# Performance work log

Hardware: AMD Instinct MI355X
Metric: run time of the kernel (lower is better)

The kernel has to match this reference:

```python
import jax, jax.numpy as jnp
import numpy as np

C = 64
SIZE = 448
PATCH = 14
P2 = PATCH * PATCH                 # 196, per-chunk token count
SPLIT = (SIZE * SIZE) // P2        # 1024 chunks
TG = PATCH * 4                     # 56, pooled global resolution
POOL = SIZE // TG                  # 8, exact avg-pool factor
EPS = 1e-5


def setup_inputs() -> dict:
    key = jax.random.key(0)
    ks = jax.random.split(key, 10)
    b = 2
    x = jax.random.normal(ks[0], (b, C, SIZE, SIZE), dtype=jnp.float32)
    s = 1.0 / np.sqrt(C)
    return {
        "x": x,
        "gn_w": jnp.ones((C,), jnp.float32),
        "gn_b": jnp.zeros((C,), jnp.float32),
        "q_w": jax.random.normal(ks[1], (C, C), jnp.float32) * s,
        "q_b": jnp.zeros((C,), jnp.float32),
        "k_w": jax.random.normal(ks[2], (C, C), jnp.float32) * s,
        "k_b": jnp.zeros((C,), jnp.float32),
        "v_w": jax.random.normal(ks[3], (C, C), jnp.float32) * s,
        "v_b": jnp.zeros((C,), jnp.float32),
        "proj_w": jax.random.normal(ks[4], (C, C), jnp.float32) * s,
    }


def _conv1x1(t, W, bias=None):
    out = jnp.einsum('oc,bchw->bohw', W, t)
    if bias is not None:
        out = out + bias[None, :, None, None]
    return out


def _group_norm(x, w, b):
    # GroupNorm(num_groups=1): normalize over (C,H,W) per sample
    mean = x.mean(axis=(1, 2, 3), keepdims=True)
    var = x.var(axis=(1, 2, 3), keepdims=True)
    xn = (x - mean) * jax.lax.rsqrt(var + EPS)
    return xn * w[None, :, None, None] + b[None, :, None, None]


def reference(x, gn_w, gn_b, q_w, q_b, k_w, k_b, v_w, v_b, proj_w):
    b, c, h, w = x.shape
    xn = _group_norm(x, gn_w, gn_b)
    q = _conv1x1(xn, q_w, q_b)
    k = _conv1x1(xn, k_w, k_b)
    v = _conv1x1(xn, v_w, v_b)

    # ---- patch-local attention (channels*chunks as feature dim S) ----
    S = c * SPLIT  # 65536
    qf = q.reshape(b, S, P2)
    kf = k.reshape(b, S, P2)
    vf = v.reshape(b, S, P2)
    wm = jnp.einsum('bsp,bsq->bpq', qf, kf) * (S ** -0.5)  # [b,196,196]
    wm = jax.nn.softmax(wm, axis=2)
    # h[b,s,q'] = sum_k v[b,s,k] * wm[b,q',k]
    hp = jnp.einsum('bsk,bqk->bsq', vf, wm).reshape(b, c, h, w)

    # ---- global pooled attention ----
    pool = lambda t: t.reshape(b, c, TG, POOL, TG, POOL).mean(axis=(3, 5))
    qg = pool(q).reshape(b, c, TG * TG)
    kg = pool(k).reshape(b, c, TG * TG)
    vg = pool(v).reshape(b, c, TG * TG)
    wg = jnp.einsum('bcp,bcq->bpq', qg, kg) * (c ** -0.5)  # [b,3136,3136]
    wg = jax.nn.softmax(wg, axis=2)
    hg = jnp.einsum('bck,bqk->bcq', vg, wg).reshape(b, c, TG, TG)
    hg = jnp.repeat(jnp.repeat(hg, POOL, axis=2), POOL, axis=3)

    h_in = 0.75 * hp + 0.25 * hg
    out = _conv1x1(h_in, proj_w)  # proj_out, no bias
    return x + out
```

## Files before the change

### kernel.cpp

```cpp
#include <hip/hip_runtime.h>

#define NB 2
#define NC 64
#define HW 200704
#define CHW 12845056
#define P2 196
#define NCHUNK 1024
#define NCELL 3136
#define WMN 38416

typedef __attribute__((ext_vector_type(8))) short bfrag;
typedef __attribute__((ext_vector_type(4))) float ffrag;
typedef __attribute__((ext_vector_type(4))) short short4v;
typedef __attribute__((ext_vector_type(4))) float float4v;

#define MFMA16(A,B,C) __builtin_amdgcn_mfma_f32_16x16x32_bf16(A,B,C,0,0,0)

__device__ __forceinline__ short f2bf(float f) {
  unsigned u = __builtin_bit_cast(unsigned, f);
  u = u + 0x7FFFu + ((u >> 16) & 1u);
  return (short)(u >> 16);
}

__global__ __launch_bounds__(256) void k0_fold(
    const float* __restrict__ pw, const float* __restrict__ vw,
    const float* __restrict__ vb, float* __restrict__ wtld, float* __restrict__ btld) {
  int t = threadIdx.x;
  if (blockIdx.x == 0) {
    #pragma unroll
    for (int i = 0; i < 16; ++i) {
      int idx = i*256 + t;
      int o = idx >> 6, c = idx & 63;
      float s = 0.f;
      for (int m = 0; m < 64; ++m) s += pw[o*64 + m] * vw[m*64 + c];
      wtld[o*64 + c] = s;
    }
  } else {
    if (t < 64) {
      float s = 0.f;
      for (int m = 0; m < 64; ++m) s += pw[t*64 + m] * vb[m];
      btld[t] = s;
    }
  }
}

__global__ __launch_bounds__(64) void k1_stats_pool(
    const float* __restrict__ x, float* __restrict__ xpool, float* __restrict__ partials) {
  int bx = blockIdx.x;
  int batch = bx / (64*56);
  int c = (bx / 56) % 64;
  int pr = bx % 56;
  int l = threadIdx.x;
  const float* xp = x + (size_t)batch*CHW + (size_t)c*HW + pr*8*448;
  float cell = 0.f, s2 = 0.f;
  if (l < 56) {
    #pragma unroll
    for (int r = 0; r < 8; ++r) {
      float4v a = *(const float4v*)(xp + r*448 + l*8);
      float4v b = *(const float4v*)(xp + r*448 + l*8 + 4);
      #pragma unroll
      for (int j = 0; j < 4; ++j) { cell += a[j] + b[j]; s2 += a[j]*a[j] + b[j]*b[j]; }
    }
    xpool[((size_t)batch*64 + c)*NCELL + pr*56 + l] = cell * (1.f/64.f);
  }
  float s1 = (l < 56) ? cell : 0.f;
  #pragma unroll
  for (int m = 1; m < 64; m <<= 1) { s1 += __shfl_xor(s1, m, 64); s2 += __shfl_xor(s2, m, 64); }
  if (l == 0) { partials[bx*2] = s1; partials[bx*2 + 1] = s2; }
}

__global__ __launch_bounds__(256) void k1b_reduce(
    const float* __restrict__ partials, float* __restrict__ stats) {
  __shared__ float red[2][256];
  int t = threadIdx.x;
  for (int b = 0; b < NB; ++b) {
    float s1 = 0.f, s2 = 0.f;
    for (int i = t; i < 3584; i += 256) {
      s1 += partials[(b*3584 + i)*2];
      s2 += partials[(b*3584 + i)*2 + 1];
    }
    red[0][t] = s1; red[1][t] = s2;
    __syncthreads();
    for (int m = 128; m > 0; m >>= 1) {
      if (t < m) { red[0][t] += red[0][t+m]; red[1][t] += red[1][t+m]; }
      __syncthreads();
    }
    if (t == 0) { stats[b*2] = red[0][0]; stats[b*2+1] = red[1][0]; }
    __syncthreads();
  }
}

__global__ __launch_bounds__(256) void k2_qkv(
    const float* __restrict__ x, const float* __restrict__ gnw, const float* __restrict__ gnb,
    const float* __restrict__ qw, const float* __restrict__ qb,
    const float* __restrict__ kw, const float* __restrict__ kb,
    const float* __restrict__ vw, const float* __restrict__ vb,
    const float* __restrict__ stats,
    short* __restrict__ qx, short* __restrict__ kx, short* __restrict__ vnat) {
  __shared__ __attribute__((aligned(16))) short xnt[256*72];
  int bx = blockIdx.x;
  int batch = bx / 784;
  int px0 = (bx % 784) * 256;
  int t = threadIdx.x;
  float s1 = stats[batch*2], s2 = stats[batch*2+1];
  float mean = s1 * (1.f/CHW);
  float rstd = rsqrtf(s2*(1.f/CHW) - mean*mean + 1e-5f);
  for (int it = 0; it < 64; it += 4) {
    float vv[4];
    #pragma unroll
    for (int r = 0; r < 4; ++r) {
      float v = x[(size_t)batch*CHW + (size_t)(it+r)*HW + px0 + t];
      vv[r] = (v - mean) * rstd * gnw[it+r] + gnb[it+r];
    }
    short4v s;
    #pragma unroll
    for (int r = 0; r < 4; ++r) s[r] = f2bf(vv[r]);
    *(short4v*)(xnt + t*72 + it) = s;
  }
  __syncthreads();
  int l = t & 63, w = t >> 6, li = l & 15, q_ = l >> 4;
  bfrag bfr[4][2];
  #pragma unroll
  for (int nn = 0; nn < 4; ++nn) {
    int row = (w*4 + nn)*16 + li;
    bfr[nn][0] = *(const bfrag*)(xnt + row*72 + q_*8);
    bfr[nn][1] = *(const bfrag*)(xnt + row*72 + 32 + q_*8);
  }
  const float* Ws[3] = {qw, kw, vw};
  const float* Bs[3] = {qb, kb, vb};
  for (int T = 0; T < 3; ++T) {
    ffrag acc[4][4];
    #pragma unroll
    for (int mt = 0; mt < 4; ++mt) {
      bfrag a0, a1;
      const float* wp = Ws[T] + (mt*16 + li)*64;
      #pragma unroll
      for (int j = 0; j < 8; ++j) { a0[j] = f2bf(wp[q_*8 + j]); a1[j] = f2bf(wp[32 + q_*8 + j]); }
      #pragma unroll
      for (int nn = 0; nn < 4; ++nn) {
        ffrag z = {0.f,0.f,0.f,0.f};
        z = MFMA16(a0, bfr[nn][0], z);
        z = MFMA16(a1, bfr[nn][1], z);
        acc[mt][nn] = z;
      }
    }
    if (T < 2) {
      short* dstb = (T == 0 ? qx : kx) + (size_t)batch*HW*64;
      #pragma unroll
      for (int nn = 0; nn < 4; ++nn) {
        int px = px0 + (w*4 + nn)*16 + li;
        #pragma unroll
        for (int mt = 0; mt < 4; ++mt) {
          float4v bias = *(const float4v*)(Bs[T] + mt*16 + q_*4);
          short4v s;
          #pragma unroll
          for (int r = 0; r < 4; ++r) s[r] = f2bf(acc[mt][nn][r] + bias[r]);
          *(short4v*)(dstb + (size_t)px*64 + mt*16 + q_*4) = s;
        }
      }
    } else {
      #pragma unroll
      for (int nn = 0; nn < 4; ++nn) {
        int px = px0 + (w*4 + nn)*16 + li;
        #pragma unroll
        for (int mt = 0; mt < 4; ++mt) {
          float4v bias = *(const float4v*)(Bs[T] + mt*16 + q_*4);
          #pragma unroll
          for (int r = 0; r < 4; ++r) {
            int c = mt*16 + q_*4 + r;
            vnat[((size_t)batch*64 + c)*HW + px] = f2bf(acc[mt][nn][r] + bias[r]);
          }
        }
      }
    }
  }
}

__global__ __launch_bounds__(256) void k2a_pool_qkv(
    const float* __restrict__ xpool, const float* __restrict__ stats,
    const float* __restrict__ gnw, const float* __restrict__ gnb,
    const float* __restrict__ qw, const float* __restrict__ qb,
    const float* __restrict__ kw, const float* __restrict__ kb,
    const float* __restrict__ vw, const float* __restrict__ vb,
    short* __restrict__ qgt, short* __restrict__ kgt, short* __restrict__ vgn) {
  __shared__ float xs[64][64];
  int bx = blockIdx.x;
  int batch = bx / 49;
  int j0 = (bx % 49) * 64;
  int t = threadIdx.x;
  float s1 = stats[batch*2], s2 = stats[batch*2+1];
  float mean = s1 * (1.f/CHW);
  float rstd = rsqrtf(s2*(1.f/CHW) - mean*mean + 1e-5f);
  #pragma unroll
  for (int it = 0; it < 16; ++it) {
    int idx = t + it*256;
    int c = idx >> 6, jl = idx & 63;
    float v = xpool[((size_t)batch*64 + c)*NCELL + j0 + jl];
    xs[c][jl] = (v - mean)*rstd*gnw[c] + gnb[c];
  }
  __syncthreads();
  int jl = t & 63;
  int og = (t >> 6) * 16;
  int j = j0 + jl;
  for (int T = 0; T < 3; ++T) {
    const float* W  = (T==0 ? qw : (T==1 ? kw : vw));
    const float* Bv = (T==0 ? qb : (T==1 ? kb : vb));
    float o16[16];
    #pragma unroll
    for (int oo = 0; oo < 16; ++oo) o16[oo] = Bv[og+oo];
    for (int c = 0; c < 64; ++c) {
      float xv = xs[c][jl];
      #pragma unroll
      for (int oo = 0; oo < 16; ++oo) o16[oo] += W[(og+oo)*64 + c] * xv;
    }
    if (T < 2) {
      short* dst = (T==0 ? qgt : kgt) + ((size_t)batch*NCELL + j)*64 + og;
      #pragma unroll
      for (int oo = 0; oo < 16; oo += 4) {
        short4v s;
        #pragma unroll
        for (int r = 0; r < 4; ++r) s[r] = f2bf(o16[oo+r]);
        *(short4v*)(dst + oo) = s;
      }
    } else {
      #pragma unroll
      for (int oo = 0; oo < 16; ++oo)
        vgn[((size_t)batch*64 + og + oo)*NCELL + j] = f2bf(o16[oo]);
    }
  }
}

__global__ __launch_bounds__(512) void k3_wm(
    const short* __restrict__ qx, const short* __restrict__ kx, float* __restrict__ wmacc) {
  int bx = blockIdx.x;
  int batch = bx >> 6;
  int slab = bx & 63;
  int t = threadIdx.x;
  int l = t & 63, w = t >> 6, li = l & 15, q_ = l >> 4;
  int wm_ = w >> 2, wn = w & 3;
  int m0 = wm_ * 7, mcnt = wm_ ? 6 : 7;
  int nt0 = wn ? 4 + (wn-1)*3 : 0, ncnt = wn ? 3 : 4;
  ffrag acc[7][4];
  #pragma unroll
  for (int i = 0; i < 7; ++i)
    #pragma unroll
    for (int j = 0; j < 4; ++j) acc[i][j] = (ffrag){0.f,0.f,0.f,0.f};
  const short* qbase = qx + (size_t)batch*HW*64;
  const short* kbase = kx + (size_t)batch*HW*64;
  for (int c8 = 0; c8 < 16; ++c8) {
    int chunk = slab*16 + c8;
    const short* qc = qbase + (size_t)chunk*P2*64;
    const short* kc = kbase + (size_t)chunk*P2*64;
    #pragma unroll
    for (int ks = 0; ks < 2; ++ks) {
      int koff = ks*32 + q_*8;
      bfrag af[7], bf[4];
      #pragma unroll
      for (int mi = 0; mi < 7; ++mi) if (mi < mcnt)
        af[mi] = *(const bfrag*)(qc + (size_t)((m0+mi)*16 + li)*64 + koff);
      #pragma unroll
      for (int ni = 0; ni < 4; ++ni) if (ni < ncnt)
        bf[ni] = *(const bfrag*)(kc + (size_t)((nt0+ni)*16 + li)*64 + koff);
      #pragma unroll
      for (int mi = 0; mi < 7; ++mi) if (mi < mcnt)
        #pragma unroll
        for (int ni = 0; ni < 4; ++ni) if (ni < ncnt)
          acc[mi][ni] = MFMA16(af[mi], bf[ni], acc[mi][ni]);
    }
  }
  float* wdst = wmacc + (size_t)batch*WMN;
  #pragma unroll
  for (int mi = 0; mi < 7; ++mi) if (mi < mcnt)
    #pragma unroll
    for (int ni = 0; ni < 4; ++ni) if (ni < ncnt) {
      int qcol = (nt0+ni)*16 + li;
      if (qcol < 196)
        #pragma unroll
        for (int r = 0; r < 4; ++r) {
          int prow = (m0+mi)*16 + q_*4 + r;
          if (prow < 196) atomicAdd(wdst + prow*196 + qcol, acc[mi][ni][r]);
        }
    }
}

__global__ __launch_bounds__(64) void k4_softmax(
    const float* __restrict__ wmacc, short* __restrict__ P) {
  int bx = blockIdx.x;
  int batch = bx / 208;
  int p = bx % 208;
  int l = threadIdx.x;
  short* prow = P + ((size_t)batch*208 + p)*224;
  if (p >= 196) { for (int j = l; j < 224; j += 64) prow[j] = 0; return; }
  const float* src = wmacc + (size_t)batch*WMN + p*196;
  float v[4]; float mx = -1e30f;
  #pragma unroll
  for (int i = 0; i < 4; ++i) {
    int q = l + i*64;
    v[i] = (q < 196) ? src[q]*(1.f/256.f) : -1e30f;
    mx = fmaxf(mx, v[i]);
  }
  #pragma unroll
  for (int m = 1; m < 64; m <<= 1) mx = fmaxf(mx, __shfl_xor(mx, m, 64));
  float s = 0.f;
  #pragma unroll
  for (int i = 0; i < 4; ++i) { v[i] = __expf(v[i] - mx); s += v[i]; }
  #pragma unroll
  for (int m = 1; m < 64; m <<= 1) s += __shfl_xor(s, m, 64);
  float inv = 0.75f / s;
  #pragma unroll
  for (int i = 0; i < 4; ++i) {
    int q = l + i*64;
    if (q < 224) prow[q] = (q < 196) ? f2bf(v[i]*inv) : (short)0;
  }
}

__global__ __launch_bounds__(256) void k5_gattn(
    const short* __restrict__ qgt, const short* __restrict__ kgt,
    const short* __restrict__ vgn, float* __restrict__ hgt) {
  __shared__ __attribute__((aligned(16))) short Pl[4][16][72];
  __shared__ __attribute__((aligned(16))) float alph[4][16];
  __shared__ __attribute__((aligned(16))) float Om[4][16][64];
  __shared__ __attribute__((aligned(16))) float ml[4][2][16];
  int bx = blockIdx.x;
  int batch = bx / 196;
  int i0 = (bx % 196) * 16;
  int t = threadIdx.x;
  int w = t >> 6, l = t & 63, li = l & 15, q_ = l >> 4;
  const short* qg = qgt + (size_t)batch*NCELL*64;
  const short* kg = kgt + (size_t)batch*NCELL*64;
  const short* vg = vgn + (size_t)batch*64*NCELL;
  bfrag bq0 = *(const bfrag*)(qg + (size_t)(i0+li)*64 + q_*8);
  bfrag bq1 = *(const bfrag*)(qg + (size_t)(i0+li)*64 + 32 + q_*8);
  float m_run = -1e30f, l_run = 0.f;
  ffrag oa[4];
  #pragma unroll
  for (int i = 0; i < 4; ++i) oa[i] = (ffrag){0.f,0.f,0.f,0.f};
  for (int jt = w; jt < 49; jt += 4) {
    int j0 = jt*64;
    ffrag st[4];
    #pragma unroll
    for (int mt = 0; mt < 4; ++mt) {
      bfrag a0 = *(const bfrag*)(kg + (size_t)(j0 + mt*16 + li)*64 + q_*8);
      bfrag a1 = *(const bfrag*)(kg + (size_t)(j0 + mt*16 + li)*64 + 32 + q_*8);
      ffrag z = {0.f,0.f,0.f,0.f};
      z = MFMA16(a0, bq0, z);
      z = MFMA16(a1, bq1, z);
      st[mt] = z;
    }
    float mx = -1e30f;
    #pragma unroll
    for (int mt = 0; mt < 4; ++mt)
      #pragma unroll
      for (int r = 0; r < 4; ++r) { st[mt][r] *= 0.125f; mx = fmaxf(mx, st[mt][r]); }
    mx = fmaxf(mx, __shfl_xor(mx, 16, 64));
    mx = fmaxf(mx, __shfl_xor(mx, 32, 64));
    float m_new = fmaxf(m_run, mx);
    float alpha = __expf(m_run - m_new);
    float ps = 0.f;
    short4v pk[4];
    #pragma unroll
    for (int mt = 0; mt < 4; ++mt)
      #pragma unroll
      for (int r = 0; r < 4; ++r) { float e = __expf(st[mt][r] - m_new); ps += e; pk[mt][r] = f2bf(e); }
    ps += __shfl_xor(ps, 16, 64);
    ps += __shfl_xor(ps, 32, 64);
    l_run = l_run*alpha + ps;
    m_run = m_new;
    #pragma unroll
    for (int mt = 0; mt < 4; ++mt) *(short4v*)(&Pl[w][li][mt*16 + q_*4]) = pk[mt];
    alph[w][li] = alpha;
    float4v al = *(const float4v*)(&alph[w][q_*4]);
    #pragma unroll
    for (int nt = 0; nt < 4; ++nt)
      #pragma unroll
      for (int r = 0; r < 4; ++r) oa[nt][r] *= al[r];
    #pragma unroll
    for (int ks = 0; ks < 2; ++ks) {
      bfrag a = *(const bfrag*)(&Pl[w][li][ks*32 + q_*8]);
      #pragma unroll
      for (int nt = 0; nt < 4; ++nt) {
        bfrag b = *(const bfrag*)(vg + (size_t)(nt*16 + li)*NCELL + j0 + ks*32 + q_*8);
        oa[nt] = MFMA16(a, b, oa[nt]);
      }
    }
  }
  ml[w][0][li] = m_run;
  ml[w][1][li] = l_run;
  #pragma unroll
  for (int nt = 0; nt < 4; ++nt)
    #pragma unroll
    for (int r = 0; r < 4; ++r)
      Om[w][q_*4 + r][nt*16 + li] = oa[nt][r];
  __syncthreads();
  int qq = t >> 4, c4 = (t & 15) * 4;
  float m0 = ml[0][0][qq], m1 = ml[1][0][qq], m2 = ml[2][0][qq], m3 = ml[3][0][qq];
  float ms = fmaxf(fmaxf(m0, m1), fmaxf(m2, m3));
  float s0 = __expf(m0 - ms), s1 = __expf(m1 - ms);
  float s2 = __expf(m2 - ms), s3 = __expf(m3 - ms);
  float lt = ml[0][1][qq]*s0 + ml[1][1][qq]*s1 + ml[2][1][qq]*s2 + ml[3][1][qq]*s3;
  float inv = 1.f / lt;
  float sw[4] = {s0, s1, s2, s3};
  float4v o = {0.f, 0.f, 0.f, 0.f};
  #pragma unroll
  for (int w2 = 0; w2 < 4; ++w2) {
    float4v ov = *(const float4v*)(&Om[w2][qq][c4]);
    #pragma unroll
    for (int r = 0; r < 4; ++r) o[r] += ov[r] * sw[w2];
  }
  float4v outv;
  #pragma unroll
  for (int r = 0; r < 4; ++r) outv[r] = o[r] * inv;
  *(float4v*)(hgt + (size_t)batch*NCELL*64 + (size_t)(i0 + qq)*64 + c4) = outv;
}

__global__ __launch_bounds__(256) void k6_hp_out(
    const short* __restrict__ vtld, const short* __restrict__ P,
    const float* __restrict__ hgt,
    const float* __restrict__ x, float* __restrict__ out) {
  __shared__ __attribute__((aligned(16))) short smem[64*232];
  short* vch = smem;
  short* fsb = smem;
  int bx = blockIdx.x;
  int batch = bx >> 10;
  int chunk = bx & 1023;
  int t = threadIdx.x;
  const short* vsrc = vtld + (size_t)batch*64*HW + chunk*P2;
  for (int idx = t; idx < 3136; idx += 256) {
    int c = idx / 49, po = idx % 49;
    *(short4v*)(vch + c*232 + po*4) = *(const short4v*)(vsrc + (size_t)c*HW + po*4);
  }
  for (int idx = t; idx < 448; idx += 256) {
    int c = idx / 7, po = idx % 7;
    *(short4v*)(vch + c*232 + 196 + po*4) = (short4v){0,0,0,0};
  }
  __syncthreads();
  int l = t & 63, w = t >> 6, li = l & 15, q_ = l >> 4;
  int nt0 = w ? 4 + (w-1)*3 : 0;
  int ncnt = w ? 3 : 4;
  const short* Pb = P + (size_t)batch*208*224;
  ffrag acc[4][4];
  #pragma unroll
  for (int i = 0; i < 4; ++i)
    #pragma unroll
    for (int j = 0; j < 4; ++j) acc[i][j] = (ffrag){0.f,0.f,0.f,0.f};
  #pragma unroll
  for (int ks = 0; ks < 7; ++ks) {
    int koff = ks*32 + q_*8;
    bfrag av[4];
    #pragma unroll
    for (int mt = 0; mt < 4; ++mt) av[mt] = *(const bfrag*)(vch + (mt*16 + li)*232 + koff);
    #pragma unroll
    for (int ni = 0; ni < 4; ++ni) if (ni < ncnt) {
      bfrag bp = *(const bfrag*)(Pb + (size_t)((nt0+ni)*16 + li)*224 + koff);
      #pragma unroll
      for (int mt = 0; mt < 4; ++mt) acc[mt][ni] = MFMA16(av[mt], bp, acc[mt][ni]);
    }
  }
  __syncthreads();
  #pragma unroll
  for (int ni = 0; ni < 4; ++ni) if (ni < ncnt) {
    int pp = (nt0+ni)*16 + li;
    if (pp < 196) {
      #pragma unroll
      for (int mt = 0; mt < 4; ++mt)
        #pragma unroll
        for (int r = 0; r < 4; ++r)
          fsb[(mt*16 + q_*4 + r)*204 + pp] = f2bf(acc[mt][ni][r]);
    }
  }
  __syncthreads();
  const float* hgb = hgt + (size_t)batch*NCELL*64;
  const float* xb = x + (size_t)batch*CHW;
  float* ob = out + (size_t)batch*CHW;
  int gbase = chunk*P2;
  for (int idx = t; idx < 3136; idx += 256) {
    int c = idx / 49, po = idx % 49;
    int g = gbase + po*4;
    int cell = ((g/448) >> 3)*56 + ((g%448) >> 3);
    float hr = 0.25f * hgb[cell*64 + c];
    size_t off = (size_t)c*HW + (size_t)gbase + po*4;
    float4v xv = *(const float4v*)(xb + off);
    short4v fb = *(const short4v*)(fsb + c*204 + po*4);
    float4v o;
    #pragma unroll
    for (int r = 0; r < 4; ++r) {
      float fv = __builtin_bit_cast(float, ((unsigned)(unsigned short)fb[r]) << 16);
      o[r] = xv[r] + fv + hr;
    }
    *(float4v*)(ob + off) = o;
  }
}

extern "C" void kernel_launch(void* const* d_in, const int* in_sizes, int n_in,
                              void* d_out, int out_size, void* d_ws, size_t ws_size,
                              hipStream_t stream) {
  (void)in_sizes; (void)n_in; (void)out_size; (void)ws_size;
  const float* x   = (const float*)d_in[0];
  const float* gnw = (const float*)d_in[1];
  const float* gnb = (const float*)d_in[2];
  const float* qw  = (const float*)d_in[3];
  const float* qb  = (const float*)d_in[4];
  const float* kw  = (const float*)d_in[5];
  const float* kb  = (const float*)d_in[6];
  const float* vw  = (const float*)d_in[7];
  const float* vb  = (const float*)d_in[8];
  const float* pw  = (const float*)d_in[9];
  float* out = (float*)d_out;
  char* ws = (char*)d_ws;

  short* qx    = (short*)(ws + 0);
  short* kx    = (short*)(ws + 51380224);
  short* vnat  = (short*)(ws + 102760448);
  float* xpool = (float*)(ws + 154140672);
  short* qgt   = (short*)(ws + 155746304);
  short* kgt   = (short*)(ws + 156549120);
  short* vgn   = (short*)(ws + 157351936);
  float* hgt   = (float*)(ws + 158154752);
  short* P     = (short*)(ws + 159760384);
  float* wmacc = (float*)(ws + 159946752);
  float* stats = (float*)(ws + 160254080);
  float* partials = (float*)(ws + 159760384);
  float* wtld = (float*)(ws + 158154752);
  float* btld = (float*)(ws + 158154752 + 16384);

  hipMemsetAsync(ws + 159946752, 0, 307328, stream);
  k0_fold      <<<dim3(2),        dim3(256), 0, stream>>>(pw, vw, vb, wtld, btld);
  k1_stats_pool<<<dim3(NB*64*56), dim3(64),  0, stream>>>(x, xpool, partials);
  k1b_reduce   <<<dim3(1),        dim3(256), 0, stream>>>(partials, stats);
  k2_qkv       <<<dim3(NB*784),   dim3(256), 0, stream>>>(x, gnw, gnb, qw, qb, kw, kb, wtld, btld, stats, qx, kx, vnat);
  k2a_pool_qkv <<<dim3(NB*49),    dim3(256), 0, stream>>>(xpool, stats, gnw, gnb, qw, qb, kw, kb, wtld, btld, qgt, kgt, vgn);
  k3_wm        <<<dim3(NB*64),    dim3(512), 0, stream>>>(qx, kx, wmacc);
  k4_softmax   <<<dim3(NB*208),   dim3(64),  0, stream>>>(wmacc, P);
  k5_gattn     <<<dim3(NB*196),   dim3(256), 0, stream>>>(qgt, kgt, vgn, hgt);
  k6_hp_out    <<<dim3(NB*1024),  dim3(256), 0, stream>>>(vnat, P, hgt, x, out);
}
```

Measured before the change: 596.3 us.

## Fold GroupNorm into per-batch bf16 QKV weights and vectorize V stores

```diff
diff --git a/kernel.cpp b/kernel.cpp
--- a/kernel.cpp
+++ b/kernel.cpp
@@ -90,31 +90,55 @@
   }
 }
 
-__global__ __launch_bounds__(256) void k2_qkv(
-    const float* __restrict__ x, const float* __restrict__ gnw, const float* __restrict__ gnb,
+__global__ __launch_bounds__(256) void k0b_foldgn(
+    const float* __restrict__ stats, const float* __restrict__ gnw, const float* __restrict__ gnb,
     const float* __restrict__ qw, const float* __restrict__ qb,
     const float* __restrict__ kw, const float* __restrict__ kb,
     const float* __restrict__ vw, const float* __restrict__ vb,
-    const float* __restrict__ stats,
-    short* __restrict__ qx, short* __restrict__ kx, short* __restrict__ vnat) {
-  __shared__ __attribute__((aligned(16))) short xnt[256*72];
-  int bx = blockIdx.x;
-  int batch = bx / 784;
-  int px0 = (bx % 784) * 256;
+    short* __restrict__ qwb, short* __restrict__ kwb, short* __restrict__ vwb,
+    float* __restrict__ qbb, float* __restrict__ kbb, float* __restrict__ vbb) {
+  __shared__ float a_s[64], d_s[64];
+  int batch = blockIdx.x;
   int t = threadIdx.x;
   float s1 = stats[batch*2], s2 = stats[batch*2+1];
   float mean = s1 * (1.f/CHW);
   float rstd = rsqrtf(s2*(1.f/CHW) - mean*mean + 1e-5f);
+  if (t < 64) { float a = rstd*gnw[t]; a_s[t] = a; d_s[t] = gnb[t] - mean*a; }
+  __syncthreads();
+  const float* Ws[3] = {qw, kw, vw};
+  const float* Bs[3] = {qb, kb, vb};
+  short* Wo[3] = {qwb, kwb, vwb};
+  float* Bo[3] = {qbb, kbb, vbb};
+  for (int T = 0; T < 3; ++T) {
+    #pragma unroll
+    for (int i = 0; i < 16; ++i) {
+      int idx = i*256 + t;
+      int c = idx & 63;
+      Wo[T][batch*4096 + idx] = f2bf(Ws[T][idx] * a_s[c]);
+    }
+    if (t < 64) {
+      float s = Bs[T][t];
+      for (int c = 0; c < 64; ++c) s += Ws[T][t*64 + c] * d_s[c];
+      Bo[T][batch*64 + t] = s;
+    }
+  }
+}
+
+__global__ __launch_bounds__(256) void k2_qkv(
+    const float* __restrict__ x,
+    const short* __restrict__ qwb, const short* __restrict__ kwb, const short* __restrict__ vwb,
+    const float* __restrict__ qbb, const float* __restrict__ kbb, const float* __restrict__ vbb,
+    short* __restrict__ qx, short* __restrict__ kx, short* __restrict__ vnat) {
+  __shared__ __attribute__((aligned(16))) short xnt[256*72];
+  int bx = blockIdx.x;
+  int batch = bx / 784;
+  int px0 = (bx % 784) * 256;
+  int t = threadIdx.x;
   for (int it = 0; it < 64; it += 4) {
-    float vv[4];
-    #pragma unroll
-    for (int r = 0; r < 4; ++r) {
-      float v = x[(size_t)batch*CHW + (size_t)(it+r)*HW + px0 + t];
-      vv[r] = (v - mean) * rstd * gnw[it+r] + gnb[it+r];
-    }
     short4v s;
     #pragma unroll
-    for (int r = 0; r < 4; ++r) s[r] = f2bf(vv[r]);
+    for (int r = 0; r < 4; ++r)
+      s[r] = f2bf(x[(size_t)batch*CHW + (size_t)(it+r)*HW + px0 + t]);
     *(short4v*)(xnt + t*72 + it) = s;
   }
   __syncthreads();
@@ -126,21 +150,24 @@
     bfr[nn][0] = *(const bfrag*)(xnt + row*72 + q_*8);
     bfr[nn][1] = *(const bfrag*)(xnt + row*72 + 32 + q_*8);
   }
-  const float* Ws[3] = {qw, kw, vw};
-  const float* Bs[3] = {qb, kb, vb};
+  const short* Wb[3] = {qwb + batch*4096, kwb + batch*4096, vwb + batch*4096};
+  const float* Bb[3] = {qbb + batch*64, kbb + batch*64, vbb + batch*64};
   for (int T = 0; T < 3; ++T) {
     ffrag acc[4][4];
     #pragma unroll
     for (int mt = 0; mt < 4; ++mt) {
-      bfrag a0, a1;
-      const float* wp = Ws[T] + (mt*16 + li)*64;
-      #pragma unroll
-      for (int j = 0; j < 8; ++j) { a0[j] = f2bf(wp[q_*8 + j]); a1[j] = f2bf(wp[32 + q_*8 + j]); }
+      bfrag aw0 = *(const bfrag*)(Wb[T] + (mt*16 + li)*64 + q_*8);
+      bfrag aw1 = *(const bfrag*)(Wb[T] + (mt*16 + li)*64 + 32 + q_*8);
       #pragma unroll
       for (int nn = 0; nn < 4; ++nn) {
         ffrag z = {0.f,0.f,0.f,0.f};
-        z = MFMA16(a0, bfr[nn][0], z);
-        z = MFMA16(a1, bfr[nn][1], z);
+        if (T < 2) {
+          z = MFMA16(aw0, bfr[nn][0], z);
+          z = MFMA16(aw1, bfr[nn][1], z);
+        } else {
+          z = MFMA16(bfr[nn][0], aw0, z);
+          z = MFMA16(bfr[nn][1], aw1, z);
+        }
         acc[mt][nn] = z;
       }
     }
@@ -151,7 +178,7 @@
         int px = px0 + (w*4 + nn)*16 + li;
         #pragma unroll
         for (int mt = 0; mt < 4; ++mt) {
-          float4v bias = *(const float4v*)(Bs[T] + mt*16 + q_*4);
+          float4v bias = *(const float4v*)(Bb[T] + mt*16 + q_*4);
           short4v s;
           #pragma unroll
           for (int r = 0; r < 4; ++r) s[r] = f2bf(acc[mt][nn][r] + bias[r]);
@@ -160,16 +187,15 @@
       }
     } else {
       #pragma unroll
-      for (int nn = 0; nn < 4; ++nn) {
-        int px = px0 + (w*4 + nn)*16 + li;
+      for (int mt = 0; mt < 4; ++mt) {
+        float bias = Bb[2][mt*16 + li];
+        short* vrow = vnat + ((size_t)batch*64 + mt*16 + li)*HW + px0;
         #pragma unroll
-        for (int mt = 0; mt < 4; ++mt) {
-          float4v bias = *(const float4v*)(Bs[T] + mt*16 + q_*4);
+        for (int nn = 0; nn < 4; ++nn) {
+          short4v s;
           #pragma unroll
-          for (int r = 0; r < 4; ++r) {
-            int c = mt*16 + q_*4 + r;
-            vnat[((size_t)batch*64 + c)*HW + px] = f2bf(acc[mt][nn][r] + bias[r]);
-          }
+          for (int r = 0; r < 4; ++r) s[r] = f2bf(acc[mt][nn][r] + bias);
+          *(short4v*)(vrow + (w*4 + nn)*16 + q_*4) = s;
         }
       }
     }
@@ -522,12 +548,19 @@
   float* partials = (float*)(ws + 159760384);
   float* wtld = (float*)(ws + 158154752);
   float* btld = (float*)(ws + 158154752 + 16384);
+  short* qwb  = (short*)(ws + 158154752 + 32768);
+  short* kwb  = (short*)(ws + 158154752 + 49152);
+  short* vwb  = (short*)(ws + 158154752 + 65536);
+  float* qbb  = (float*)(ws + 158154752 + 81920);
+  float* kbb  = (float*)(ws + 158154752 + 82432);
+  float* vbb  = (float*)(ws + 158154752 + 82944);
 
   hipMemsetAsync(ws + 159946752, 0, 307328, stream);
   k0_fold      <<<dim3(2),        dim3(256), 0, stream>>>(pw, vw, vb, wtld, btld);
   k1_stats_pool<<<dim3(NB*64*56), dim3(64),  0, stream>>>(x, xpool, partials);
   k1b_reduce   <<<dim3(1),        dim3(256), 0, stream>>>(partials, stats);
-  k2_qkv       <<<dim3(NB*784),   dim3(256), 0, stream>>>(x, gnw, gnb, qw, qb, kw, kb, wtld, btld, stats, qx, kx, vnat);
+  k0b_foldgn   <<<dim3(NB),       dim3(256), 0, stream>>>(stats, gnw, gnb, qw, qb, kw, kb, wtld, btld, qwb, kwb, vwb, qbb, kbb, vbb);
+  k2_qkv       <<<dim3(NB*784),   dim3(256), 0, stream>>>(x, qwb, kwb, vwb, qbb, kbb, vbb, qx, kx, vnat);
   k2a_pool_qkv <<<dim3(NB*49),    dim3(256), 0, stream>>>(xpool, stats, gnw, gnb, qw, qb, kw, kb, wtld, btld, qgt, kgt, vgn);
   k3_wm        <<<dim3(NB*64),    dim3(512), 0, stream>>>(qx, kx, wmacc);
   k4_softmax   <<<dim3(NB*208),   dim3(64),  0, stream>>>(wmacc, P);
```

Result: no change. 599.9 us (+0.6%).
